# Performance work log

Hardware: AMD Instinct MI355X
Metric: run time of the kernel (lower is better)

## Reference

```python
import jax, jax.numpy as jnp
import numpy as np
import math

N_EMBED = 2048
N_HEAD = 16
HEAD_DIM = N_EMBED // N_HEAD  # 128
ROPE_BASE = 10000.0


def _rope_tables(T, dim, dtype):
    # inv_freq over even indices, emb = concat(freqs, freqs) along last dim
    inv_freq = 1.0 / (ROPE_BASE ** (jnp.arange(0, dim, 2, dtype=jnp.float32) / dim))
    t = jnp.arange(T, dtype=jnp.float32)
    freqs = jnp.einsum('i,j->ij', t, inv_freq)          # [T, dim/2]
    emb = jnp.concatenate([freqs, freqs], axis=-1)      # [T, dim]
    return jnp.cos(emb).astype(dtype), jnp.sin(emb).astype(dtype)


def _rotate_half(x):
    h = x.shape[-1] // 2
    return jnp.concatenate([-x[..., h:], x[..., :h]], axis=-1)


def setup_inputs() -> dict:
    key = jax.random.key(0)
    ks = jax.random.split(key, 5)
    B, T, C = 32, 256, N_EMBED
    s = 1.0 / math.sqrt(C)
    return {
        'x': jax.random.normal(ks[0], (B, T, C), dtype=jnp.float32),
        'wq': jax.random.normal(ks[1], (C, C), dtype=jnp.float32) * s,
        'wk': jax.random.normal(ks[2], (C, C), dtype=jnp.float32) * s,
        'wv': jax.random.normal(ks[3], (C, C), dtype=jnp.float32) * s,
        'wo': jax.random.normal(ks[4], (C, C), dtype=jnp.float32) * s,
    }


def reference(x, wq, wk, wv, wo):
    B, T, C = x.shape
    H, D = N_HEAD, HEAD_DIM
    # torch Linear: y = x @ W^T
    q = (x @ wq.T).reshape(B, T, H, D).transpose(0, 2, 1, 3)  # [B,H,T,D]
    k = (x @ wk.T).reshape(B, T, H, D).transpose(0, 2, 1, 3)
    v = (x @ wv.T).reshape(B, T, H, D).transpose(0, 2, 1, 3)

    cos, sin = _rope_tables(T, D, x.dtype)  # [T,D] each, broadcast over B,H
    q = q * cos + _rotate_half(q) * sin
    k = k * cos + _rotate_half(k) * sin

    att = jnp.einsum('bhqd,bhkd->bhqk', q, k) / math.sqrt(D)
    causal = jnp.triu(jnp.ones((T, T), dtype=bool), k=1)
    att = jnp.where(causal, jnp.finfo(att.dtype).min, att)
    att = jax.nn.softmax(att, axis=-1)
    # dropout p=0.0 -> identity
    y = jnp.einsum('bhqk,bhkd->bhqd', att, v)
    y = y.transpose(0, 2, 1, 3).reshape(B, T, C)
    return y @ wo.T
```

## Files before the change

kernel.cpp:

```cpp
#include <hip/hip_runtime.h>

#define HB 32
#define HT 256
#define HC 2048
#define HH 16
#define HD 128
#define HM (HB * HT)

typedef __bf16 bf16x8 __attribute__((ext_vector_type(8)));
typedef float f32x4 __attribute__((ext_vector_type(4)));

__device__ __forceinline__ unsigned short f2bf(float f) {
  unsigned u = __float_as_uint(f);
  u += 0x7FFFu + ((u >> 16) & 1u);
  return (unsigned short)(u >> 16);
}

__global__ __launch_bounds__(256) void cvt_all(
    const float* __restrict__ x, const float* __restrict__ wq, const float* __restrict__ wk,
    const float* __restrict__ wv, const float* __restrict__ wo,
    unsigned short* __restrict__ xb, unsigned short* __restrict__ wqb,
    unsigned short* __restrict__ wkb, unsigned short* __restrict__ wvb,
    unsigned short* __restrict__ wob) {
  size_t i = (size_t)blockIdx.x * 256 + threadIdx.x;
  const float* src;
  unsigned short* dst;
  size_t off;
  if (i < 4194304) {
    src = x; dst = xb; off = i;
  } else {
    size_t j = i - 4194304;
    int w = (int)(j >> 20);
    off = j & 1048575;
    src = (w == 0) ? wq : (w == 1) ? wk : (w == 2) ? wv : wo;
    dst = (w == 0) ? wqb : (w == 1) ? wkb : (w == 2) ? wvb : wob;
  }
  float4 v = ((const float4*)src)[off];
  ushort4 o;
  o.x = f2bf(v.x); o.y = f2bf(v.y); o.z = f2bf(v.z); o.w = f2bf(v.w);
  ((ushort4*)dst)[off] = o;
}

__device__ __forceinline__ void gl_lds16(const unsigned short* g, unsigned short* l) {
  __builtin_amdgcn_global_load_lds((const __attribute__((address_space(1))) void*)g,
                                   (__attribute__((address_space(3))) void*)l, 16, 0, 0);
}

__device__ __forceinline__ int nfcol(int wn, int nf) {
  return (wn >> 1) * 128 + (wn & 1) * 32 + (nf & 1) * 16 + (nf >> 1) * 64;
}

__device__ __forceinline__ void stage32(const unsigned short* __restrict__ src,
                                        unsigned short* dst, int tid) {
#pragma unroll
  for (int i = 0; i < 2; i++) {
    int c = i * 512 + tid;
    int row = c >> 2, slot = c & 3;
    int gc = slot ^ (row & 3);
    gl_lds16(src + (size_t)row * HC + gc * 8, dst + c * 8);
  }
}

#define KT 64

__device__ __forceinline__ void gemm_core8(const unsigned short* __restrict__ A,
                                           const unsigned short* __restrict__ W,
                                           unsigned short* lsA, unsigned short* lsB,
                                           f32x4 acc[8][4], int tid) {
  const int lane = tid & 63, l16 = lane & 15, quad = lane >> 4;
  const int wave = tid >> 6, wm = wave >> 2, wn = wave & 3;

  stage32(A, lsA, tid);
  stage32(W, lsB, tid);
  stage32(A + 32, lsA + 8192, tid);
  stage32(W + 32, lsB + 8192, tid);
  stage32(A + 64, lsA + 16384, tid);
  stage32(W + 64, lsB + 16384, tid);
  asm volatile("s_waitcnt vmcnt(8)");
  __builtin_amdgcn_s_barrier();

  for (int t = 0; t < KT; ++t) {
    const unsigned short* cA = lsA + (t & 3) * 8192;
    const unsigned short* cB = lsB + (t & 3) * 8192;
    unsigned short* nA = lsA + ((t + 3) & 3) * 8192;
    unsigned short* nB = lsB + ((t + 3) & 3) * 8192;
    const bool pf = (t + 3 < KT);
#pragma unroll
    for (int ph = 0; ph < 2; ++ph) {
      bf16x8 af[4], bfv[4];
#pragma unroll
      for (int mf = 0; mf < 4; ++mf) {
        int row = wm * 128 + ph * 64 + mf * 16 + l16;
        int ch = quad ^ (row & 3);
        af[mf] = *(const bf16x8*)(cA + row * 32 + ch * 8);
      }
#pragma unroll
      for (int nf = 0; nf < 4; ++nf) {
        int row = nfcol(wn, nf) + l16;
        int ch = quad ^ (row & 3);
        bfv[nf] = *(const bf16x8*)(cB + row * 32 + ch * 8);
      }
      if (pf) {
        if (ph == 0) stage32(A + (size_t)(t + 3) * 32, nA, tid);
        else         stage32(W + (size_t)(t + 3) * 32, nB, tid);
      }
      if (ph == 1) {
        const int rem = KT - 2 - t;
        if (rem >= 2)      asm volatile("s_waitcnt vmcnt(8)");
        else if (rem == 1) asm volatile("s_waitcnt vmcnt(4)");
        else if (rem == 0) asm volatile("s_waitcnt vmcnt(0)");
      }
      __builtin_amdgcn_s_barrier();
      __builtin_amdgcn_s_setprio(1);
#pragma unroll
      for (int mf = 0; mf < 4; ++mf)
#pragma unroll
        for (int nf = 0; nf < 4; ++nf)
          acc[ph * 4 + mf][nf] =
              __builtin_amdgcn_mfma_f32_16x16x32_bf16(af[mf], bfv[nf], acc[ph * 4 + mf][nf], 0, 0, 0);
      __builtin_amdgcn_s_setprio(0);
      __builtin_amdgcn_s_barrier();
    }
  }
}

__global__ __launch_bounds__(512, 2) void gemm_out(const unsigned short* __restrict__ A,
                                                   const unsigned short* __restrict__ W,
                                                   float* __restrict__ outp) {
  __shared__ __align__(16) unsigned short lsA[32768];
  __shared__ __align__(16) unsigned short lsB[32768];
  const int tid = threadIdx.x;
  const int lane = tid & 63, wave = tid >> 6;
  const int l16 = lane & 15, quad = lane >> 4;
  const int wm = wave >> 2, wn = wave & 3;
  const int bm = blockIdx.x, bn = blockIdx.y;

  f32x4 acc[8][4];
#pragma unroll
  for (int i = 0; i < 8; i++)
#pragma unroll
    for (int j = 0; j < 4; j++) acc[i][j] = f32x4{0.f, 0.f, 0.f, 0.f};

  gemm_core8(A + (size_t)bm * 256 * HC, W + (size_t)bn * 256 * HC, lsA, lsB, acc, tid);

#pragma unroll
  for (int mf = 0; mf < 8; mf++)
#pragma unroll
    for (int nf = 0; nf < 4; nf++) {
      const int n = bn * 256 + nfcol(wn, nf) + l16;
#pragma unroll
      for (int r = 0; r < 4; r++) {
        const int m = bm * 256 + wm * 128 + mf * 16 + quad * 4 + r;
        outp[(size_t)m * HC + n] = acc[mf][nf][r];
      }
    }
}

__global__ __launch_bounds__(512, 2) void gemm_qkv(const unsigned short* __restrict__ A,
                                                   const unsigned short* __restrict__ W0,
                                                   const unsigned short* __restrict__ W1,
                                                   const unsigned short* __restrict__ W2,
                                                   unsigned short* __restrict__ Qo,
                                                   unsigned short* __restrict__ Ko,
                                                   unsigned short* __restrict__ Vto) {
  __shared__ __align__(16) unsigned short lsA[32768];
  __shared__ __align__(16) unsigned short lsB[32768];
  const int tid = threadIdx.x;
  const int lane = tid & 63, wave = tid >> 6;
  const int l16 = lane & 15, quad = lane >> 4;
  const int wm = wave >> 2, wn = wave & 3;
  const int bm = blockIdx.x;
  const int which = blockIdx.y >> 3;
  const int bn = blockIdx.y & 7;

  f32x4 acc[8][4];
#pragma unroll
  for (int i = 0; i < 8; i++)
#pragma unroll
    for (int j = 0; j < 4; j++) acc[i][j] = f32x4{0.f, 0.f, 0.f, 0.f};

  if (which < 2) {
    const unsigned short* W = (which == 0) ? W0 : W1;
    unsigned short* outp = (which == 0) ? Qo : Ko;
    gemm_core8(A + (size_t)bm * 256 * HC, W + (size_t)bn * 256 * HC, lsA, lsB, acc, tid);
    const int h = bn * 2 + (wn >> 1);
#pragma unroll
    for (int p = 0; p < 2; p++) {
      const int d = (wn & 1) * 32 + p * 16 + l16;
      const float invf = __expf((float)d * (-0.14391156831212787f));
#pragma unroll
      for (int mf = 0; mf < 8; mf++)
#pragma unroll
        for (int r = 0; r < 4; r++) {
          const int m = bm * 256 + wm * 128 + mf * 16 + quad * 4 + r;
          const int t = m & 255, b = m >> 8;
          float ang = (float)t * invf;
          float sn, cs;
          __sincosf(ang, &sn, &cs);
          float lo = acc[mf][p][r], hi = acc[mf][p + 2][r];
          size_t base = (((size_t)b * HH + h) * HT + t) * HD;
          outp[base + d] = f2bf(lo * cs - hi * sn);
          outp[base + 64 + d] = f2bf(hi * cs + lo * sn);
        }
    }
  } else {
    const int tok = bm;
    const int ch = bn;
    gemm_core8(W2 + (size_t)ch * 256 * HC, A + (size_t)tok * 256 * HC, lsA, lsB, acc, tid);
#pragma unroll
    for (int mf = 0; mf < 8; mf++)
#pragma unroll
      for (int nf = 0; nf < 4; nf++) {
        const int tcol = nfcol(wn, nf) + l16;
#pragma unroll
        for (int r = 0; r < 4; r++) {
          const int cabs = ch * 256 + wm * 128 + mf * 16 + quad * 4 + r;
          const int hh = cabs >> 7, d = cabs & 127;
          Vto[(((size_t)tok * HH + hh) * HD + d) * HT + tcol] = f2bf(acc[mf][nf][r]);
        }
      }
  }
}

__global__ __launch_bounds__(256) void attn_kernel(const unsigned short* __restrict__ Q,
                                                   const unsigned short* __restrict__ K,
                                                   const unsigned short* __restrict__ Vt,
                                                   unsigned short* __restrict__ Y) {
  const int g = blockIdx.x;
  const int wq = 3 - (g >> 9);
  const int bh = g & 511;
  const int wave = threadIdx.x >> 6;
  const int lane = threadIdx.x & 63;
  const int quad = lane >> 4, l16 = lane & 15;

  const unsigned short* Qh = Q + (size_t)bh * HT * HD;
  const unsigned short* Kh = K + (size_t)bh * HT * HD;
  const unsigned short* Vh = Vt + (size_t)bh * HD * HT;

  __shared__ __align__(16) unsigned short P[4][16 * 72];
  unsigned short* Pw = P[wave];

  const int qrow = wq * 64 + wave * 16;

  bf16x8 qf[4];
#pragma unroll
  for (int ks = 0; ks < 4; ks++)
    qf[ks] = *(const bf16x8*)(Qh + (size_t)(qrow + l16) * HD + ks * 32 + quad * 8);

  f32x4 o[8];
#pragma unroll
  for (int di = 0; di < 8; di++) o[di] = f32x4{0.f, 0.f, 0.f, 0.f};
  float mrow[4], lrow[4];
#pragma unroll
  for (int r = 0; r < 4; r++) { mrow[r] = -1e30f; lrow[r] = 0.f; }

  const float scale = 0.088388347648318447f;

  for (int ct = 0; ct <= wq; ++ct) {
    f32x4 s[4];
#pragma unroll
    for (int ni = 0; ni < 4; ni++) s[ni] = f32x4{0.f, 0.f, 0.f, 0.f};
    const int nimax = (ct == wq) ? wave : 3;
#pragma unroll
    for (int ks = 0; ks < 4; ks++) {
#pragma unroll
      for (int ni = 0; ni < 4; ni++) {
        if (ni <= nimax) {
          bf16x8 kf = *(const bf16x8*)(Kh + (size_t)(ct * 64 + ni * 16 + l16) * HD + ks * 32 + quad * 8);
          s[ni] = __builtin_amdgcn_mfma_f32_16x16x32_bf16(qf[ks], kf, s[ni], 0, 0, 0);
        }
      }
    }
    if (ct == wq) {
#pragma unroll
      for (int ni = 0; ni < 4; ni++)
#pragma unroll
        for (int r = 0; r < 4; r++) {
          int qr = wave * 16 + quad * 4 + r;
          int kc = ni * 16 + l16;
          s[ni][r] = (kc <= qr) ? s[ni][r] * scale : -1e30f;
        }
    } else {
#pragma unroll
      for (int ni = 0; ni < 4; ni++)
#pragma unroll
        for (int r = 0; r < 4; r++) s[ni][r] *= scale;
    }
#pragma unroll
    for (int r = 0; r < 4; r++) {
      float v = fmaxf(fmaxf(s[0][r], s[1][r]), fmaxf(s[2][r], s[3][r]));
      v = fmaxf(v, __shfl_xor(v, 1, 64));
      v = fmaxf(v, __shfl_xor(v, 2, 64));
      v = fmaxf(v, __shfl_xor(v, 4, 64));
      v = fmaxf(v, __shfl_xor(v, 8, 64));
      float mnew = fmaxf(mrow[r], v);
      float alpha = __expf(mrow[r] - mnew);
      mrow[r] = mnew;
      float rs = 0.f;
#pragma unroll
      for (int ni = 0; ni < 4; ni++) {
        float e = __expf(s[ni][r] - mnew);
        s[ni][r] = e;
        rs += e;
      }
      rs += __shfl_xor(rs, 1, 64);
      rs += __shfl_xor(rs, 2, 64);
      rs += __shfl_xor(rs, 4, 64);
      rs += __shfl_xor(rs, 8, 64);
      lrow[r] = lrow[r] * alpha + rs;
#pragma unroll
      for (int di = 0; di < 8; di++) o[di][r] *= alpha;
    }
#pragma unroll
    for (int ni = 0; ni < 4; ni++)
#pragma unroll
      for (int r = 0; r < 4; r++)
        Pw[(quad * 4 + r) * 72 + ni * 16 + l16] = f2bf(s[ni][r]);
#pragma unroll
    for (int ks = 0; ks < 2; ks++) {
      bf16x8 pf = *(const bf16x8*)(Pw + (size_t)l16 * 72 + ks * 32 + quad * 8);
#pragma unroll
      for (int di = 0; di < 8; di++) {
        bf16x8 vf = *(const bf16x8*)(Vh + (size_t)(di * 16 + l16) * HT + ct * 64 + ks * 32 + quad * 8);
        o[di] = __builtin_amdgcn_mfma_f32_16x16x32_bf16(pf, vf, o[di], 0, 0, 0);
      }
    }
  }

  const int b = bh >> 4, h = bh & 15;
#pragma unroll
  for (int r = 0; r < 4; r++) {
    float inv = 1.f / lrow[r];
    int t = qrow + quad * 4 + r;
    size_t rowb = ((size_t)b * HT + t) * HC + h * HD;
#pragma unroll
    for (int di = 0; di < 8; di++)
      Y[rowb + di * 16 + l16] = f2bf(o[di][r] * inv);
  }
}

extern "C" void kernel_launch(void* const* d_in, const int* in_sizes, int n_in,
                              void* d_out, int out_size, void* d_ws, size_t ws_size,
                              hipStream_t stream) {
  const float* x  = (const float*)d_in[0];
  const float* wq = (const float*)d_in[1];
  const float* wk = (const float*)d_in[2];
  const float* wv = (const float*)d_in[3];
  const float* wo = (const float*)d_in[4];
  float* out = (float*)d_out;

  char* ws = (char*)d_ws;
  const size_t MB = (size_t)1 << 20;
  unsigned short* wqb = (unsigned short*)(ws + 0 * MB);
  unsigned short* wkb = (unsigned short*)(ws + 8 * MB);
  unsigned short* wvb = (unsigned short*)(ws + 16 * MB);
  unsigned short* wob = (unsigned short*)(ws + 24 * MB);
  unsigned short* xb  = (unsigned short*)(ws + 32 * MB);
  unsigned short* Qb  = (unsigned short*)(ws + 64 * MB);
  unsigned short* Kb  = (unsigned short*)(ws + 96 * MB);
  unsigned short* Vtb = (unsigned short*)(ws + 128 * MB);
  unsigned short* Yb  = xb;

  cvt_all<<<32768, 256, 0, stream>>>(x, wq, wk, wv, wo, xb, wqb, wkb, wvb, wob);

  gemm_qkv<<<dim3(HM / 256, 24), 512, 0, stream>>>(xb, wqb, wkb, wvb, Qb, Kb, Vtb);

  attn_kernel<<<2048, 256, 0, stream>>>(Qb, Kb, Vtb, Yb);

  gemm_out<<<dim3(HM / 256, HC / 256), 512, 0, stream>>>(Yb, wob, out);
}
```

Measured before the change: 545.9 us.

## Pair causal query tiles per block, batch K/V loads, lazy softmax rescale, new LDS swizzle

The attention kernel now gives each block two complementary query tiles (3+0 and 2+1), so every block does the same amount of causal work, and the grid is halved. K fragments are loaded in batches ahead of the MFMAs, and the first half of the V fragments is prefetched before the softmax. The online softmax skips the max/rescale update unless the new max exceeds the old one by more than 8, cutting exp and multiply work but letting exponentials grow up to e^8 before renormalising. Separately, the GEMM LDS swizzle changes to use (row>>1)&3 with a per-lane hoisted offset, meant to reduce bank conflicts.

```diff
diff --git a/kernel.cpp b/kernel.cpp
--- a/kernel.cpp
+++ b/kernel.cpp
@@ -56,7 +56,7 @@
   for (int i = 0; i < 2; i++) {
     int c = i * 512 + tid;
     int row = c >> 2, slot = c & 3;
-    int gc = slot ^ (row & 3);
+    int gc = slot ^ ((row >> 1) & 3);
     gl_lds16(src + (size_t)row * HC + gc * 8, dst + c * 8);
   }
 }
@@ -69,6 +69,7 @@
                                            f32x4 acc[8][4], int tid) {
   const int lane = tid & 63, l16 = lane & 15, quad = lane >> 4;
   const int wave = tid >> 6, wm = wave >> 2, wn = wave & 3;
+  const int ch8 = (quad ^ ((l16 >> 1) & 3)) * 8;
 
   stage32(A, lsA, tid);
   stage32(W, lsB, tid);
@@ -91,14 +92,12 @@
 #pragma unroll
       for (int mf = 0; mf < 4; ++mf) {
         int row = wm * 128 + ph * 64 + mf * 16 + l16;
-        int ch = quad ^ (row & 3);
-        af[mf] = *(const bf16x8*)(cA + row * 32 + ch * 8);
+        af[mf] = *(const bf16x8*)(cA + row * 32 + ch8);
       }
 #pragma unroll
       for (int nf = 0; nf < 4; ++nf) {
         int row = nfcol(wn, nf) + l16;
-        int ch = quad ^ (row & 3);
-        bfv[nf] = *(const bf16x8*)(cB + row * 32 + ch * 8);
+        bfv[nf] = *(const bf16x8*)(cB + row * 32 + ch8);
       }
       if (pf) {
         if (ph == 0) stage32(A + (size_t)(t + 3) * 32, nA, tid);
@@ -227,8 +226,8 @@
                                                    const unsigned short* __restrict__ Vt,
                                                    unsigned short* __restrict__ Y) {
   const int g = blockIdx.x;
-  const int wq = 3 - (g >> 9);
   const int bh = g & 511;
+  const int pairp = g >> 9;
   const int wave = threadIdx.x >> 6;
   const int lane = threadIdx.x & 63;
   const int quad = lane >> 4, l16 = lane & 15;
@@ -240,102 +239,138 @@
   __shared__ __align__(16) unsigned short P[4][16 * 72];
   unsigned short* Pw = P[wave];
 
-  const int qrow = wq * 64 + wave * 16;
-
-  bf16x8 qf[4];
-#pragma unroll
-  for (int ks = 0; ks < 4; ks++)
-    qf[ks] = *(const bf16x8*)(Qh + (size_t)(qrow + l16) * HD + ks * 32 + quad * 8);
-
-  f32x4 o[8];
-#pragma unroll
-  for (int di = 0; di < 8; di++) o[di] = f32x4{0.f, 0.f, 0.f, 0.f};
-  float mrow[4], lrow[4];
-#pragma unroll
-  for (int r = 0; r < 4; r++) { mrow[r] = -1e30f; lrow[r] = 0.f; }
-
   const float scale = 0.088388347648318447f;
-
-  for (int ct = 0; ct <= wq; ++ct) {
-    f32x4 s[4];
-#pragma unroll
-    for (int ni = 0; ni < 4; ni++) s[ni] = f32x4{0.f, 0.f, 0.f, 0.f};
-    const int nimax = (ct == wq) ? wave : 3;
-#pragma unroll
-    for (int ks = 0; ks < 4; ks++) {
-#pragma unroll
-      for (int ni = 0; ni < 4; ni++) {
-        if (ni <= nimax) {
-          bf16x8 kf = *(const bf16x8*)(Kh + (size_t)(ct * 64 + ni * 16 + l16) * HD + ks * 32 + quad * 8);
-          s[ni] = __builtin_amdgcn_mfma_f32_16x16x32_bf16(qf[ks], kf, s[ni], 0, 0, 0);
+  const int b = bh >> 4, h = bh & 15;
+
+  for (int half = 0; half < 2; ++half) {
+    const int wq = (pairp == 0) ? (half == 0 ? 3 : 0) : (half == 0 ? 2 : 1);
+    const int qrow = wq * 64 + wave * 16;
+
+    bf16x8 qf[4];
+#pragma unroll
+    for (int ks = 0; ks < 4; ks++)
+      qf[ks] = *(const bf16x8*)(Qh + (size_t)(qrow + l16) * HD + ks * 32 + quad * 8);
+
+    f32x4 o[8];
+#pragma unroll
+    for (int di = 0; di < 8; di++) o[di] = f32x4{0.f, 0.f, 0.f, 0.f};
+    float mrow[4], lrow[4];
+#pragma unroll
+    for (int r = 0; r < 4; r++) { mrow[r] = -1e30f; lrow[r] = 0.f; }
+
+    for (int ct = 0; ct <= wq; ++ct) {
+      f32x4 s[4];
+#pragma unroll
+      for (int ni = 0; ni < 4; ni++) s[ni] = f32x4{0.f, 0.f, 0.f, 0.f};
+      const int nimax = (ct == wq) ? wave : 3;
+#pragma unroll
+      for (int ksh = 0; ksh < 2; ksh++) {
+        bf16x8 kf[4][2];
+#pragma unroll
+        for (int ni = 0; ni < 4; ni++)
+          if (ni <= nimax)
+#pragma unroll
+            for (int k2 = 0; k2 < 2; k2++)
+              kf[ni][k2] = *(const bf16x8*)(Kh + (size_t)(ct * 64 + ni * 16 + l16) * HD +
+                                            (ksh * 2 + k2) * 32 + quad * 8);
+#pragma unroll
+        for (int k2 = 0; k2 < 2; k2++)
+#pragma unroll
+          for (int ni = 0; ni < 4; ni++)
+            if (ni <= nimax)
+              s[ni] = __builtin_amdgcn_mfma_f32_16x16x32_bf16(qf[ksh * 2 + k2], kf[ni][k2],
+                                                              s[ni], 0, 0, 0);
+      }
+      bf16x8 vf0[8];
+#pragma unroll
+      for (int di = 0; di < 8; di++)
+        vf0[di] = *(const bf16x8*)(Vh + (size_t)(di * 16 + l16) * HT + ct * 64 + quad * 8);
+
+      if (ct == wq) {
+#pragma unroll
+        for (int ni = 0; ni < 4; ni++)
+#pragma unroll
+          for (int r = 0; r < 4; r++) {
+            int qr = wave * 16 + quad * 4 + r;
+            int kc = ni * 16 + l16;
+            s[ni][r] = (kc <= qr) ? s[ni][r] * scale : -1e30f;
+          }
+      } else {
+#pragma unroll
+        for (int ni = 0; ni < 4; ni++)
+#pragma unroll
+          for (int r = 0; r < 4; r++) s[ni][r] *= scale;
+      }
+      float pm[4];
+#pragma unroll
+      for (int r = 0; r < 4; r++) {
+        float v = fmaxf(fmaxf(s[0][r], s[1][r]), fmaxf(s[2][r], s[3][r]));
+        v = fmaxf(v, __shfl_xor(v, 1, 64));
+        v = fmaxf(v, __shfl_xor(v, 2, 64));
+        v = fmaxf(v, __shfl_xor(v, 4, 64));
+        v = fmaxf(v, __shfl_xor(v, 8, 64));
+        pm[r] = v;
+      }
+      float ex = fmaxf(fmaxf(pm[0] - mrow[0], pm[1] - mrow[1]),
+                       fmaxf(pm[2] - mrow[2], pm[3] - mrow[3]));
+      ex = fmaxf(ex, __shfl_xor(ex, 16, 64));
+      ex = fmaxf(ex, __shfl_xor(ex, 32, 64));
+      if (ex > 8.f) {
+#pragma unroll
+        for (int r = 0; r < 4; r++) {
+          float mnew = fmaxf(mrow[r], pm[r]);
+          float alpha = __expf(mrow[r] - mnew);
+          mrow[r] = mnew;
+          lrow[r] *= alpha;
+#pragma unroll
+          for (int di = 0; di < 8; di++) o[di][r] *= alpha;
         }
       }
+#pragma unroll
+      for (int r = 0; r < 4; r++) {
+        float rs = 0.f;
+#pragma unroll
+        for (int ni = 0; ni < 4; ni++) {
+          float e = __expf(s[ni][r] - mrow[r]);
+          s[ni][r] = e;
+          rs += e;
+        }
+        rs += __shfl_xor(rs, 1, 64);
+        rs += __shfl_xor(rs, 2, 64);
+        rs += __shfl_xor(rs, 4, 64);
+        rs += __shfl_xor(rs, 8, 64);
+        lrow[r] += rs;
+      }
+#pragma unroll
+      for (int ni = 0; ni < 4; ni++)
+#pragma unroll
+        for (int r = 0; r < 4; r++)
+          Pw[(quad * 4 + r) * 72 + ni * 16 + l16] = f2bf(s[ni][r]);
+      {
+        bf16x8 pf = *(const bf16x8*)(Pw + (size_t)l16 * 72 + quad * 8);
+#pragma unroll
+        for (int di = 0; di < 8; di++)
+          o[di] = __builtin_amdgcn_mfma_f32_16x16x32_bf16(pf, vf0[di], o[di], 0, 0, 0);
+      }
+      {
+        bf16x8 pf = *(const bf16x8*)(Pw + (size_t)l16 * 72 + 32 + quad * 8);
+#pragma unroll
+        for (int di = 0; di < 8; di++) {
+          bf16x8 vf = *(const bf16x8*)(Vh + (size_t)(di * 16 + l16) * HT + ct * 64 + 32 + quad * 8);
+          o[di] = __builtin_amdgcn_mfma_f32_16x16x32_bf16(pf, vf, o[di], 0, 0, 0);
+        }
+      }
     }
-    if (ct == wq) {
-#pragma unroll
-      for (int ni = 0; ni < 4; ni++)
-#pragma unroll
-        for (int r = 0; r < 4; r++) {
-          int qr = wave * 16 + quad * 4 + r;
-          int kc = ni * 16 + l16;
-          s[ni][r] = (kc <= qr) ? s[ni][r] * scale : -1e30f;
-        }
-    } else {
-#pragma unroll
-      for (int ni = 0; ni < 4; ni++)
-#pragma unroll
-        for (int r = 0; r < 4; r++) s[ni][r] *= scale;
+
+#pragma unroll
+    for (int r = 0; r < 4; r++) {
+      float inv = 1.f / lrow[r];
+      int t = qrow + quad * 4 + r;
+      size_t rowb = ((size_t)b * HT + t) * HC + h * HD;
+#pragma unroll
+      for (int di = 0; di < 8; di++)
+        Y[rowb + di * 16 + l16] = f2bf(o[di][r] * inv);
     }
-#pragma unroll
-    for (int r = 0; r < 4; r++) {
-      float v = fmaxf(fmaxf(s[0][r], s[1][r]), fmaxf(s[2][r], s[3][r]));
-      v = fmaxf(v, __shfl_xor(v, 1, 64));
-      v = fmaxf(v, __shfl_xor(v, 2, 64));
-      v = fmaxf(v, __shfl_xor(v, 4, 64));
-      v = fmaxf(v, __shfl_xor(v, 8, 64));
-      float mnew = fmaxf(mrow[r], v);
-      float alpha = __expf(mrow[r] - mnew);
-      mrow[r] = mnew;
-      float rs = 0.f;
-#pragma unroll
-      for (int ni = 0; ni < 4; ni++) {
-        float e = __expf(s[ni][r] - mnew);
-        s[ni][r] = e;
-        rs += e;
-      }
-      rs += __shfl_xor(rs, 1, 64);
-      rs += __shfl_xor(rs, 2, 64);
-      rs += __shfl_xor(rs, 4, 64);
-      rs += __shfl_xor(rs, 8, 64);
-      lrow[r] = lrow[r] * alpha + rs;
-#pragma unroll
-      for (int di = 0; di < 8; di++) o[di][r] *= alpha;
-    }
-#pragma unroll
-    for (int ni = 0; ni < 4; ni++)
-#pragma unroll
-      for (int r = 0; r < 4; r++)
-        Pw[(quad * 4 + r) * 72 + ni * 16 + l16] = f2bf(s[ni][r]);
-#pragma unroll
-    for (int ks = 0; ks < 2; ks++) {
-      bf16x8 pf = *(const bf16x8*)(Pw + (size_t)l16 * 72 + ks * 32 + quad * 8);
-#pragma unroll
-      for (int di = 0; di < 8; di++) {
-        bf16x8 vf = *(const bf16x8*)(Vh + (size_t)(di * 16 + l16) * HT + ct * 64 + ks * 32 + quad * 8);
-        o[di] = __builtin_amdgcn_mfma_f32_16x16x32_bf16(pf, vf, o[di], 0, 0, 0);
-      }
-    }
-  }
-
-  const int b = bh >> 4, h = bh & 15;
-#pragma unroll
-  for (int r = 0; r < 4; r++) {
-    float inv = 1.f / lrow[r];
-    int t = qrow + quad * 4 + r;
-    size_t rowb = ((size_t)b * HT + t) * HC + h * HD;
-#pragma unroll
-    for (int di = 0; di < 8; di++)
-      Y[rowb + di * 16 + l16] = f2bf(o[di][r] * inv);
   }
 }
 
@@ -365,7 +400,7 @@
 
   gemm_qkv<<<dim3(HM / 256, 24), 512, 0, stream>>>(xb, wqb, wkb, wvb, Qb, Kb, Vtb);
 
-  attn_kernel<<<2048, 256, 0, stream>>>(Qb, Kb, Vtb, Yb);
+  attn_kernel<<<1024, 256, 0, stream>>>(Qb, Kb, Vtb, Yb);
 
   gemm_out<<<dim3(HM / 256, HC / 256), 512, 0, stream>>>(Yb, wob, out);
 }
```

Measured after the change: 510.3 us. -6.5%, faster.
